# Optimization experiments

Hardware: AMD Instinct MI355X
Metric: run time of the kernel (lower is better)

Reference implementation:

```python
import jax, jax.numpy as jnp
from jax import lax
import numpy as np

K = 4            # prototypes per class: 3 kmeans centroids + 1 backbone
EPS = 0.1        # sinkhorn entropic regularization
MAX_ITER = 100
THRESH = 0.01
KM_ITERS = 10    # Lloyd iterations (replaces host-side sklearn KMeans)
HW = 28          # the original reshapes pred to 28x28, fixing n = 784


def setup_inputs():
    key = jax.random.key(0)
    k1, k2, k3, k4 = jax.random.split(key, 4)
    b, n, d, c = 32, HW * HW, 1024, 20
    return {
        "query": jax.random.normal(k1, (b, n, d), dtype=jnp.float32),
        "score": jax.random.uniform(k2, (b, n, c), dtype=jnp.float32),
        "label": jax.random.randint(k3, (b, c), 0, 2),
        "gt": jax.random.randint(k4, (b, HW, HW), 0, c + 1),
        "weights": jnp.array([1.0, 1.0, 0.0, -1.0], dtype=jnp.float32),
    }


def _assign(dq, cen, selfm):
    # dq [b,m,d], cen [b,c,j,d], selfm [b,c,m] float mask -> one-hot labels, counts
    x2 = jnp.sum(dq * dq, axis=-1)                                   # [b,m]
    d2 = (x2[:, None, :, None]
          - 2.0 * jnp.einsum('bmd,bcjd->bcmj', dq, cen)
          + jnp.sum(cen * cen, axis=-1)[:, :, None, :])              # [b,c,m,j]
    oh = jax.nn.one_hot(jnp.argmin(d2, axis=-1), cen.shape[2], dtype=dq.dtype) * selfm[..., None]
    return oh, oh.sum(axis=2)


def _sinkhorn(Km, u, v):
    # vectorized over the [b,c] pair grid, per-pair early exit as in the torch loop
    def cond(st):
        it, r, cc, done = st
        return (it < MAX_ITER) & jnp.logical_not(jnp.all(done))

    def body(st):
        it, r, cc, done = st
        r1 = u / jnp.einsum('bcnj,bcj->bcn', Km, cc)
        c1 = v / jnp.einsum('bcnj,bcn->bcj', Km, r1)
        err = jnp.mean(jnp.abs(r1 - r), axis=-1)                     # [b,c]
        r = jnp.where(done[..., None], r, r1)
        cc = jnp.where(done[..., None], cc, c1)
        done = done | (err < THRESH)
        return it + 1, r, cc, done

    st = (jnp.int32(0), jnp.ones_like(u), jnp.ones_like(v),
          jnp.zeros(Km.shape[:2], dtype=bool))
    _, r, cc, _ = lax.while_loop(cond, body, st)
    return r[..., :, None] * cc[..., None, :] * Km                   # [b,c,n,K]


def _forward(query, score, label, gt, weights):
    b, n, d = query.shape
    c = score.shape[2]
    dq, ds = query[:, ::2, :], score[:, ::2, :]                      # stride-2 downsample
    m = dq.shape[1]
    cls_assign = jnp.argmax(ds, axis=-1)                             # [b,m]
    sel = cls_assign[:, None, :] == jnp.arange(c)[None, :, None]     # [b,c,m]
    selfm = sel.astype(query.dtype)
    cnt = selfm.sum(-1)                                              # [b,c]
    valid = (label > 0) & (cnt >= K)

    # ---- masked Lloyd's k-means with k-1 = 3 clusters per (image, class) pair
    order = jnp.argsort((~sel).astype(jnp.int32), axis=-1)           # masked points first
    init_idx = order[..., :K - 1]                                    # [b,c,3]
    cen = dq[jnp.arange(b)[:, None, None], init_idx]                 # [b,c,3,d]

    def km_step(cen, _):
        oh, kcnt = _assign(dq, cen, selfm)
        sums = jnp.einsum('bmd,bcmj->bcjd', dq, oh)
        cen = jnp.where(kcnt[..., None] > 0,
                        sums / jnp.maximum(kcnt, 1.0)[..., None], cen)
        return cen, None

    cen, _ = lax.scan(km_step, cen, None, length=KM_ITERS)
    oh, kcnt = _assign(dq, cen, selfm)                               # final labels

    # ---- sort centroids by mean cluster score (descending)
    sm = ds.mean(axis=-1)                                            # [b,m]
    avg = jnp.where(kcnt > 0,
                    jnp.einsum('bm,bcmj->bcj', sm, oh) / jnp.maximum(kcnt, 1.0),
                    -jnp.inf)
    ordj = jnp.argsort(-avg, axis=-1)                                # [b,c,3]
    cen = jnp.take_along_axis(cen, ordj[..., None], axis=2)

    # ---- backbone prototype = mean over unselected downsampled tokens
    un = 1.0 - selfm
    backbone = jnp.einsum('bmd,bcm->bcd', dq, un) / jnp.maximum(m - cnt, 1.0)[..., None]
    protos = jnp.concatenate([cen, backbone[:, :, None, :]], axis=2)  # [b,c,4,d]

    # ---- OT between query[0] tokens and the 4 prototypes (original uses query[0] always)
    q0 = query[0]
    q0h = q0 / jnp.maximum(jnp.linalg.norm(q0, axis=-1, keepdims=True), 1e-12)
    ph = protos / jnp.maximum(jnp.linalg.norm(protos, axis=-1, keepdims=True), 1e-12)
    sim = jnp.einsum('nd,bcjd->bcnj', q0h, ph)                       # [b,c,n,4]
    Km = lax.stop_gradient(jnp.exp(-(1.0 - sim) / EPS))              # torch.no_grad
    u = jnp.full((b, c, n), 1.0 / n, dtype=query.dtype)
    v = jnp.full((b, c, K), 1.0 / K, dtype=query.dtype)
    T = lax.stop_gradient(_sinkhorn(Km, u, v))                       # [b,c,n,4]

    valid = valid & jnp.logical_not(jnp.any(jnp.isnan(T), axis=(2, 3)))
    pred = jnp.einsum('bcnj,j->bcn', T, weights)                     # [b,c,n]

    # ---- BCE vs gt masks (28x28 -> 28x28 bilinear resize is the identity)
    y = (gt.reshape(b, -1)[:, None, :] == (jnp.arange(c) + 1)[None, :, None]).astype(pred.dtype)
    p = jnp.clip(pred, 0.0, 1.0)
    bce = -(y * jnp.maximum(jnp.log(p), -100.0)
            + (1.0 - y) * jnp.maximum(jnp.log(1.0 - p), -100.0)).mean(axis=-1)  # [b,c]
    bce = jnp.where(valid, bce, 0.0)
    total_n = valid.sum().astype(pred.dtype)
    return bce.sum() / (total_n + 1e-4)


def reference(query, score, label, gt, weights):
    return _forward(query, score, label, gt, weights)
```

## Files before the change

kernel.cpp:

```cpp
#include <hip/hip_runtime.h>
#include <cmath>

#define BB 32
#define NN 784
#define MM 392
#define DD 1024
#define CC 20
#define JJ 3
#define KP 4
#define KM_ITERS 10
#define GMAX 64
#define SKK 3
#define NCOL (BB * CC * KP)

__global__ void k_cls(const float* __restrict__ score, int* __restrict__ cls,
                      float* __restrict__ sm, int* __restrict__ cnt) {
  int t = blockIdx.x * blockDim.x + threadIdx.x;
  if (t >= BB * MM) return;
  int b = t / MM, i = t - b * MM;
  const float* s = score + ((size_t)b * NN + 2 * i) * CC;
  float best = s[0]; int bi = 0; float acc = s[0];
  #pragma unroll
  for (int c = 1; c < CC; c++) { float v = s[c]; acc += v; if (v > best) { best = v; bi = c; } }
  cls[t] = bi;
  sm[t] = acc / (float)CC;
  atomicAdd(&cnt[b * CC + bi], 1);
}

__global__ void k_valid(const int* __restrict__ label, const int* __restrict__ cnt,
                        int* __restrict__ vlist, int* __restrict__ cpos, int* __restrict__ nvp) {
  __shared__ int sf[1024];
  int t = threadIdx.x;
  int flag = 0;
  if (t < BB * CC) flag = (label[t] > 0 && cnt[t] >= KP) ? 1 : 0;
  sf[t] = flag;
  __syncthreads();
  for (int off = 1; off < 1024; off <<= 1) {
    int v = sf[t];
    int add = (t >= off) ? sf[t - off] : 0;
    __syncthreads();
    sf[t] = v + add;
    __syncthreads();
  }
  if (t < BB * CC) {
    int pos = sf[t] - flag;
    cpos[t] = flag ? pos : -1;
    if (flag) vlist[pos] = t;
  }
  if (t == 0) *nvp = sf[BB * CC - 1];
}

__global__ __launch_bounds__(256) void k_csum(const float* __restrict__ query,
    const int* __restrict__ cls, float* __restrict__ classsum) {
  int b = blockIdx.x, ch = blockIdx.y;
  int tid = threadIdx.x, lane = tid & 63, wv = tid >> 6;
  __shared__ float acc[4][CC][64];
  __shared__ int s_cls[MM];
  #pragma unroll
  for (int c = 0; c < CC; c++) acc[wv][c][lane] = 0.f;
  for (int i = tid; i < MM; i += 256) s_cls[i] = cls[b * MM + i];
  __syncthreads();
  const float* qb = query + (size_t)b * NN * DD + ch * 64 + lane;
  int i0 = wv * 98;
  #pragma unroll 4
  for (int r = 0; r < 98; r++) {
    int i = i0 + r;
    float v = qb[(size_t)(2 * i) * DD];
    int cl = s_cls[i];
    acc[wv][cl][lane] += v;
  }
  __syncthreads();
  for (int cc = wv; cc < CC; cc += 4) {
    float s = acc[0][cc][lane] + acc[1][cc][lane] + acc[2][cc][lane] + acc[3][cc][lane];
    classsum[((size_t)(b * CC + cc)) * DD + ch * 64 + lane] = s;
  }
}

__global__ __launch_bounds__(512) void k_gram(
    const float* __restrict__ query, const int* __restrict__ cls,
    const int* __restrict__ cpos, const float* __restrict__ sm,
    float* __restrict__ ph) {
  int bc = blockIdx.x;
  if (cpos[bc] < 0) return;
  int b = bc / CC, c = bc - b * CC;
  int tid = threadIdx.x, lane = tid & 63, wv = tid >> 6;
  const float* qb = query + (size_t)b * NN * DD;
  __shared__ int s_wtot[8];
  __shared__ int s_list[GMAX];
  __shared__ __align__(16) float Xs[GMAX][132];
  __shared__ float Gl[GMAX][65];
  __shared__ float s_w[JJ][GMAX];
  __shared__ int s_rank[JJ];
  __shared__ float s_red2[6];

  int flag = 0;
  if (tid < MM) flag = (cls[b * MM + tid] == c) ? 1 : 0;
  unsigned long long msk = __ballot(flag);
  int wp = __popcll(msk & ((1ull << lane) - 1ull));
  if (lane == 0) s_wtot[wv] = __popcll(msk);
  __syncthreads();
  int off = 0, mtot = 0;
  #pragma unroll
  for (int w = 0; w < 8; w++) { int t = s_wtot[w]; if (w < wv) off += t; mtot += t; }
  int mc = mtot > GMAX ? GMAX : mtot;
  if (flag) { int pos = off + wp; if (pos < GMAX) s_list[pos] = tid; }
  __syncthreads();

  const float* pb[4] = {nullptr, nullptr, nullptr, nullptr};
  float* xd[4] = {nullptr, nullptr, nullptr, nullptr};
  #pragma unroll
  for (int s = 0; s < 4; s++) {
    int e = tid + s * 512;
    if (e < mc * 32) {
      pb[s] = qb + (size_t)(2 * s_list[e >> 5]) * DD + (e & 31) * 4;
      xd[s] = &Xs[e >> 5][(e & 31) * 4];
    }
  }

  int T = (mc + 1) >> 1;
  int ntile = T * (T + 1) / 2;
  int ti_[2], tj_[2];
  float a00[2], a01[2], a10[2], a11[2];
  #pragma unroll
  for (int s = 0; s < 2; s++) {
    ti_[s] = -1; tj_[s] = 0;
    a00[s] = 0.f; a01[s] = 0.f; a10[s] = 0.f; a11[s] = 0.f;
    int p = tid + s * 512;
    if (p < ntile) {
      int i = (int)floorf((sqrtf(8.0f * (float)p + 1.0f) - 1.0f) * 0.5f);
      while ((i + 1) * (i + 2) / 2 <= p) i++;
      while (i * (i + 1) / 2 > p) i--;
      ti_[s] = i; tj_[s] = p - i * (i + 1) / 2;
    }
  }

  float4 cur[4], nxt[4];
  #pragma unroll
  for (int s = 0; s < 4; s++) {
    cur[s] = make_float4(0.f, 0.f, 0.f, 0.f);
    nxt[s] = make_float4(0.f, 0.f, 0.f, 0.f);
    if (pb[s]) cur[s] = *(const float4*)(pb[s]);
  }
  for (int ch = 0; ch < 8; ch++) {
    __syncthreads();
    #pragma unroll
    for (int s = 0; s < 4; s++) if (pb[s]) *(float4*)xd[s] = cur[s];
    if (ch < 7) {
      #pragma unroll
      for (int s = 0; s < 4; s++) if (pb[s]) nxt[s] = *(const float4*)(pb[s] + (ch + 1) * 128);
    }
    __syncthreads();
    #pragma unroll
    for (int s = 0; s < 2; s++) {
      if (ti_[s] >= 0) {
        const float4* xr0 = (const float4*)&Xs[2 * ti_[s]][0];
        const float4* xr1 = (const float4*)&Xs[2 * ti_[s] + 1][0];
        const float4* xc0 = (const float4*)&Xs[2 * tj_[s]][0];
        const float4* xc1 = (const float4*)&Xs[2 * tj_[s] + 1][0];
        float s00 = 0.f, s01 = 0.f, s10 = 0.f, s11 = 0.f;
        #pragma unroll
        for (int kk = 0; kk < 32; kk++) {
          float4 u0 = xr0[kk], u1 = xr1[kk], w0 = xc0[kk], w1 = xc1[kk];
          s00 += u0.x * w0.x + u0.y * w0.y + u0.z * w0.z + u0.w * w0.w;
          s01 += u0.x * w1.x + u0.y * w1.y + u0.z * w1.z + u0.w * w1.w;
          s10 += u1.x * w0.x + u1.y * w0.y + u1.z * w0.z + u1.w * w0.w;
          s11 += u1.x * w1.x + u1.y * w1.y + u1.z * w1.z + u1.w * w1.w;
        }
        a00[s] += s00; a01[s] += s01; a10[s] += s10; a11[s] += s11;
      }
    }
    #pragma unroll
    for (int s = 0; s < 4; s++) cur[s] = nxt[s];
  }

  #pragma unroll
  for (int s = 0; s < 2; s++) {
    if (ti_[s] >= 0) {
      int r0 = 2 * ti_[s], r1 = r0 + 1, c0 = 2 * tj_[s], c1 = c0 + 1;
      if (r0 < mc && c0 < mc) { Gl[r0][c0] = a00[s]; Gl[c0][r0] = a00[s]; }
      if (r0 < mc && c1 < mc) { Gl[r0][c1] = a01[s]; Gl[c1][r0] = a01[s]; }
      if (r1 < mc && c0 < mc) { Gl[r1][c0] = a10[s]; Gl[c0][r1] = a10[s]; }
      if (r1 < mc && c1 < mc) { Gl[r1][c1] = a11[s]; Gl[c1][r1] = a11[s]; }
    }
  }
  __syncthreads();

  if (wv == 0) {
    bool act = lane < mc;
    float smv = act ? sm[b * MM + s_list[lane]] : 0.f;
    s_w[0][lane] = (lane == 0) ? 1.f : 0.f;
    s_w[1][lane] = (lane == 1) ? 1.f : 0.f;
    s_w[2][lane] = (lane == 2) ? 1.f : 0.f;
    int aj = 0, n0 = 0, n1 = 0, n2 = 0;
    for (int it = 0; it <= KM_ITERS; it++) {
      float h0 = 0.f, h1 = 0.f, h2 = 0.f;
      if (act) {
        for (int i = 0; i < mc; i++) {
          float g = Gl[lane][i];
          h0 += s_w[0][i] * g; h1 += s_w[1][i] * g; h2 += s_w[2][i] * g;
        }
      }
      float t0 = s_w[0][lane] * h0, t1 = s_w[1][lane] * h1, t2 = s_w[2][lane] * h2;
      for (int o = 1; o < 64; o <<= 1) {
        t0 += __shfl_xor(t0, o, 64); t1 += __shfl_xor(t1, o, 64); t2 += __shfl_xor(t2, o, 64);
      }
      float e0 = t0 - 2.f * h0, e1 = t1 - 2.f * h1, e2 = t2 - 2.f * h2;
      aj = 0; float bv = e0;
      if (e1 < bv) { bv = e1; aj = 1; }
      if (e2 < bv) { bv = e2; aj = 2; }
      n0 = __popcll(__ballot(act && aj == 0));
      n1 = __popcll(__ballot(act && aj == 1));
      n2 = __popcll(__ballot(act && aj == 2));
      if (it == KM_ITERS) break;
      if (act) {
        if (n0 > 0) s_w[0][lane] = (aj == 0) ? 1.f / (float)n0 : 0.f;
        if (n1 > 0) s_w[1][lane] = (aj == 1) ? 1.f / (float)n1 : 0.f;
        if (n2 > 0) s_w[2][lane] = (aj == 2) ? 1.f / (float)n2 : 0.f;
      }
    }
    float s0 = (act && aj == 0) ? smv : 0.f;
    float s1 = (act && aj == 1) ? smv : 0.f;
    float s2 = (act && aj == 2) ? smv : 0.f;
    for (int o = 1; o < 64; o <<= 1) {
      s0 += __shfl_xor(s0, o, 64); s1 += __shfl_xor(s1, o, 64); s2 += __shfl_xor(s2, o, 64);
    }
    if (lane == 0) {
      float avg[JJ];
      avg[0] = (n0 > 0) ? s0 / (float)n0 : -INFINITY;
      avg[1] = (n1 > 0) ? s1 / (float)n1 : -INFINITY;
      avg[2] = (n2 > 0) ? s2 / (float)n2 : -INFINITY;
      bool used[JJ] = {false, false, false};
      for (int s = 0; s < JJ; s++) {
        int bi = -1; float bv = 0.f;
        for (int j = 0; j < JJ; j++)
          if (!used[j] && (bi < 0 || avg[j] > bv)) { bi = j; bv = avg[j]; }
        used[bi] = true; s_rank[bi] = s;
      }
    }
  }
  __syncthreads();

  float4 a0 = make_float4(0.f, 0.f, 0.f, 0.f), a1 = make_float4(0.f, 0.f, 0.f, 0.f);
  int j = tid >> 7, q = tid & 127;
  if (tid < 384) {
    for (int g = 0; g < mc; g++) {
      float w = s_w[j][g];
      if (w != 0.f) {
        const float4* row = (const float4*)(qb + (size_t)(2 * s_list[g]) * DD);
        float4 v0 = row[q], v1 = row[q + 128];
        a0.x += w * v0.x; a0.y += w * v0.y; a0.z += w * v0.z; a0.w += w * v0.w;
        a1.x += w * v1.x; a1.y += w * v1.y; a1.z += w * v1.z; a1.w += w * v1.w;
      }
    }
    float ssq = a0.x * a0.x + a0.y * a0.y + a0.z * a0.z + a0.w * a0.w
              + a1.x * a1.x + a1.y * a1.y + a1.z * a1.z + a1.w * a1.w;
    #pragma unroll
    for (int o = 1; o < 64; o <<= 1) ssq += __shfl_xor(ssq, o, 64);
    if (lane == 0) s_red2[wv] = ssq;
  }
  __syncthreads();
  if (tid < 384) {
    float nrm = fmaxf(sqrtf(s_red2[2 * j] + s_red2[2 * j + 1]), 1e-12f);
    float4* dst = (float4*)(ph + ((size_t)bc * KP + s_rank[j]) * DD);
    float4 o0 = make_float4(a0.x / nrm, a0.y / nrm, a0.z / nrm, a0.w / nrm);
    float4 o1 = make_float4(a1.x / nrm, a1.y / nrm, a1.z / nrm, a1.w / nrm);
    dst[q] = o0; dst[q + 128] = o1;
  }
}

__global__ __launch_bounds__(256) void k_backbone(const float* __restrict__ classsum,
    const int* __restrict__ cpos, const int* __restrict__ cnt, float* __restrict__ ph) {
  int bc = blockIdx.x;
  if (cpos[bc] < 0) return;
  int b = bc / CC;
  int tid = threadIdx.x, lane = tid & 63, wv = tid >> 6;
  __shared__ float s_red[4];
  __shared__ float s_nrm;
  float4 ts = make_float4(0.f, 0.f, 0.f, 0.f);
  for (int c2 = 0; c2 < CC; c2++) {
    float4 v = *(const float4*)(classsum + ((size_t)(b * CC + c2)) * DD + tid * 4);
    ts.x += v.x; ts.y += v.y; ts.z += v.z; ts.w += v.w;
  }
  float4 cs = *(const float4*)(classsum + (size_t)bc * DD + tid * 4);
  float denom = fmaxf((float)(MM - cnt[bc]), 1.f);
  float4 v = make_float4((ts.x - cs.x) / denom, (ts.y - cs.y) / denom,
                         (ts.z - cs.z) / denom, (ts.w - cs.w) / denom);
  float pp = v.x * v.x + v.y * v.y + v.z * v.z + v.w * v.w;
  for (int o = 1; o < 64; o <<= 1) pp += __shfl_xor(pp, o, 64);
  if (lane == 0) s_red[wv] = pp;
  __syncthreads();
  if (tid == 0) s_nrm = fmaxf(sqrtf(s_red[0] + s_red[1] + s_red[2] + s_red[3]), 1e-12f);
  __syncthreads();
  float nrm = s_nrm;
  *(float4*)(ph + ((size_t)bc * KP + 3) * DD + tid * 4) =
      make_float4(v.x / nrm, v.y / nrm, v.z / nrm, v.w / nrm);
}

__global__ void k_q0h(const float* __restrict__ query, float* __restrict__ q0h) {
  int n = blockIdx.x;
  const float* src = query + (size_t)n * DD;
  float ss = 0.f;
  for (int k = threadIdx.x; k < DD; k += 64) { float v = src[k]; ss += v * v; }
  for (int o = 32; o > 0; o >>= 1) ss += __shfl_xor(ss, o, 64);
  float nrm = fmaxf(sqrtf(ss), 1e-12f);
  for (int k = threadIdx.x; k < DD; k += 64) q0h[(size_t)n * DD + k] = src[k] / nrm;
}

__global__ __launch_bounds__(256) void k_gemm(const float* __restrict__ A,
    const float* __restrict__ ph, const int* __restrict__ vlist,
    const int* __restrict__ nvp, float* __restrict__ P) {
  int nv4 = 4 * *nvp;
  int n0 = blockIdx.y * 64;
  if (n0 >= nv4) return;
  __shared__ float As[64][20];
  __shared__ float Bs[64][20];
  int tx = threadIdx.x & 15, ty = threadIdx.x >> 4;
  int m0 = blockIdx.x * 64;
  int s = blockIdx.z;
  int lrow = threadIdx.x >> 2;
  int lk = (threadIdx.x & 3) * 4;
  int brow = n0 + lrow;
  bool bval = brow < nv4;
  const float* Brow = ph;
  if (bval) {
    int bcc = brow >> 2;
    Brow = ph + ((size_t)vlist[bcc] * KP + (brow & 3)) * DD;
  }
  float acc[4][4] = {};
  int kbase = s * 352;
  int kend = (kbase + 352 < DD) ? (kbase + 352) : DD;
  for (int k0 = kbase; k0 < kend; k0 += 16) {
    int ar = m0 + lrow;
    float4 av = (ar < NN) ? *(const float4*)(A + (size_t)ar * DD + k0 + lk)
                          : make_float4(0.f, 0.f, 0.f, 0.f);
    *(float4*)&As[lrow][lk] = av;
    float4 bv = bval ? *(const float4*)(Brow + k0 + lk)
                     : make_float4(0.f, 0.f, 0.f, 0.f);
    *(float4*)&Bs[lrow][lk] = bv;
    __syncthreads();
    #pragma unroll
    for (int kk = 0; kk < 16; kk += 4) {
      float4 a4[4], b4[4];
      #pragma unroll
      for (int i = 0; i < 4; i++) a4[i] = *(const float4*)&As[ty * 4 + i][kk];
      #pragma unroll
      for (int j = 0; j < 4; j++) b4[j] = *(const float4*)&Bs[tx + 16 * j][kk];
      #pragma unroll
      for (int i = 0; i < 4; i++)
        #pragma unroll
        for (int j = 0; j < 4; j++) {
          acc[i][j] += a4[i].x * b4[j].x;
          acc[i][j] += a4[i].y * b4[j].y;
          acc[i][j] += a4[i].z * b4[j].z;
          acc[i][j] += a4[i].w * b4[j].w;
        }
    }
    __syncthreads();
  }
  #pragma unroll
  for (int j = 0; j < 4; j++) {
    int col = n0 + tx + 16 * j;
    float4 o4 = make_float4(acc[0][j], acc[1][j], acc[2][j], acc[3][j]);
    *(float4*)(P + ((size_t)s * NCOL + col) * NN + m0 + ty * 4) = o4;
  }
}

__global__ __launch_bounds__(256) void k_sink(const float* __restrict__ P,
    const int* __restrict__ cpos, const int* __restrict__ gt,
    const float* __restrict__ wts, float* __restrict__ bce, int* __restrict__ vld) {
  int bc = blockIdx.x; int b = bc / CC, c = bc - b * CC;
  int tid = threadIdx.x;
  if (cpos[bc] < 0) {
    if (tid == 0) { bce[bc] = 0.f; vld[bc] = 0; }
    return;
  }
  int p = cpos[bc];
  int lane = tid & 63, wv = tid >> 6;
  __shared__ float ccv[KP];
  __shared__ float wred[4][5];
  __shared__ float s_err;
  __shared__ int s_nan;
  float4 kv[4]; float rr[4];
  #pragma unroll
  for (int s4 = 0; s4 < 4; s4++) {
    int n = tid + 256 * s4;
    kv[s4] = make_float4(0.f, 0.f, 0.f, 0.f); rr[s4] = 1.f;
    if (n < NN) {
      float v[KP] = {0.f, 0.f, 0.f, 0.f};
      #pragma unroll
      for (int s = 0; s < SKK; s++)
        #pragma unroll
        for (int q = 0; q < KP; q++)
          v[q] += P[((size_t)s * NCOL + 4 * p + q) * NN + n];
      float4 o;
      o.x = expf(-(1.0f - v[0]) / 0.1f);
      o.y = expf(-(1.0f - v[1]) / 0.1f);
      o.z = expf(-(1.0f - v[2]) / 0.1f);
      o.w = expf(-(1.0f - v[3]) / 0.1f);
      kv[s4] = o;
    }
  }
  if (tid < KP) ccv[tid] = 1.f;
  if (tid == 0) s_nan = 0;
  __syncthreads();
  const float uu = 1.0f / (float)NN, vv = 1.0f / (float)KP;
  for (int it = 0; it < 100; it++) {
    float c0 = ccv[0], c1 = ccv[1], c2 = ccv[2], c3 = ccv[3];
    float dsum = 0.f, p0 = 0.f, p1 = 0.f, p2 = 0.f, p3 = 0.f;
    #pragma unroll
    for (int s4 = 0; s4 < 4; s4++) {
      int n = tid + 256 * s4;
      if (n < NN) {
        float4 k4 = kv[s4];
        float S = k4.x * c0 + k4.y * c1 + k4.z * c2 + k4.w * c3;
        float r1 = uu / S;
        dsum += fabsf(r1 - rr[s4]);
        rr[s4] = r1;
        p0 += k4.x * r1; p1 += k4.y * r1; p2 += k4.z * r1; p3 += k4.w * r1;
      }
    }
    for (int o = 32; o > 0; o >>= 1) {
      dsum += __shfl_down(dsum, o, 64);
      p0 += __shfl_down(p0, o, 64); p1 += __shfl_down(p1, o, 64);
      p2 += __shfl_down(p2, o, 64); p3 += __shfl_down(p3, o, 64);
    }
    if (lane == 0) { wred[wv][0] = dsum; wred[wv][1] = p0; wred[wv][2] = p1; wred[wv][3] = p2; wred[wv][4] = p3; }
    __syncthreads();
    if (tid == 0) {
      float d = 0.f, q0 = 0.f, q1 = 0.f, q2 = 0.f, q3 = 0.f;
      for (int w = 0; w < 4; w++) { d += wred[w][0]; q0 += wred[w][1]; q1 += wred[w][2]; q2 += wred[w][3]; q3 += wred[w][4]; }
      ccv[0] = vv / q0; ccv[1] = vv / q1; ccv[2] = vv / q2; ccv[3] = vv / q3;
      s_err = d / (float)NN;
    }
    __syncthreads();
    if (s_err < 0.01f) break;
  }
  float w0 = wts[0], w1 = wts[1], w2 = wts[2], w3 = wts[3];
  float cc0 = ccv[0], cc1 = ccv[1], cc2 = ccv[2], cc3 = ccv[3];
  float bsum = 0.f; int nanloc = 0;
  const int* gtb = gt + b * NN;
  #pragma unroll
  for (int s4 = 0; s4 < 4; s4++) {
    int n = tid + 256 * s4;
    if (n < NN) {
      float4 k4 = kv[s4];
      float rv = rr[s4];
      float T0 = rv * cc0 * k4.x, T1 = rv * cc1 * k4.y, T2 = rv * cc2 * k4.z, T3 = rv * cc3 * k4.w;
      if (T0 != T0 || T1 != T1 || T2 != T2 || T3 != T3) nanloc = 1;
      float pred = T0 * w0 + T1 * w1 + T2 * w2 + T3 * w3;
      float pcl = fminf(fmaxf(pred, 0.f), 1.f);
      float t = (gtb[n] == c + 1) ? fmaxf(logf(pcl), -100.f) : fmaxf(logf(1.f - pcl), -100.f);
      bsum += t;
    }
  }
  if (nanloc) s_nan = 1;
  for (int o = 32; o > 0; o >>= 1) bsum += __shfl_down(bsum, o, 64);
  if (lane == 0) wred[wv][0] = bsum;
  __syncthreads();
  if (tid == 0) {
    float tot = wred[0][0] + wred[1][0] + wred[2][0] + wred[3][0];
    if (s_nan) { bce[bc] = 0.f; vld[bc] = 0; }
    else { bce[bc] = -(tot / (float)NN); vld[bc] = 1; }
  }
}

__global__ void k_final(const float* __restrict__ bce, const int* __restrict__ vld,
                        float* __restrict__ out) {
  __shared__ float rs[256];
  __shared__ float rc[256];
  float s = 0.f, cv = 0.f;
  for (int t = threadIdx.x; t < BB * CC; t += 256) { s += bce[t]; cv += (float)vld[t]; }
  rs[threadIdx.x] = s; rc[threadIdx.x] = cv; __syncthreads();
  for (int o = 128; o > 0; o >>= 1) {
    if (threadIdx.x < o) { rs[threadIdx.x] += rs[threadIdx.x + o]; rc[threadIdx.x] += rc[threadIdx.x + o]; }
    __syncthreads();
  }
  if (threadIdx.x == 0) out[0] = rs[0] / (rc[0] + 0.0001f);
}

extern "C" void kernel_launch(void* const* d_in, const int* in_sizes, int n_in,
                              void* d_out, int out_size, void* d_ws, size_t ws_size,
                              hipStream_t stream) {
  (void)in_sizes; (void)n_in; (void)out_size; (void)ws_size;
  const float* query = (const float*)d_in[0];
  const float* score = (const float*)d_in[1];
  const int*   label = (const int*)d_in[2];
  const int*   gt    = (const int*)d_in[3];
  const float* wts   = (const float*)d_in[4];
  float* ws = (float*)d_ws;

  size_t off = 0;
  int* cls = (int*)(ws + off);       off += (size_t)BB * MM;
  int* cnt = (int*)(ws + off);       off += (size_t)BB * CC;
  float* sm = ws + off;              off += (size_t)BB * MM;
  int* vlist = (int*)(ws + off);     off += (size_t)BB * CC;
  int* cpos = (int*)(ws + off);      off += (size_t)BB * CC;
  int* nvp = (int*)(ws + off);       off += 16;
  float* classsum = ws + off;        off += (size_t)BB * CC * DD;
  float* ph = ws + off;              off += (size_t)BB * CC * KP * DD;
  float* q0h = ws + off;             off += (size_t)NN * DD;
  float* P = ws + off;               off += (size_t)SKK * NN * NCOL;
  float* bce = ws + off;             off += (size_t)BB * CC;
  int* vld = (int*)(ws + off);       off += (size_t)BB * CC;

  hipMemsetAsync(cnt, 0, (size_t)BB * CC * sizeof(int), stream);
  k_cls<<<(BB * MM + 255) / 256, 256, 0, stream>>>(score, cls, sm, cnt);
  k_valid<<<1, 1024, 0, stream>>>(label, cnt, vlist, cpos, nvp);
  k_csum<<<dim3(BB, 16), 256, 0, stream>>>(query, cls, classsum);
  k_gram<<<BB * CC, 512, 0, stream>>>(query, cls, cpos, sm, ph);
  k_backbone<<<BB * CC, 256, 0, stream>>>(classsum, cpos, cnt, ph);
  k_q0h<<<NN, 64, 0, stream>>>(query, q0h);
  dim3 gg((NN + 63) / 64, (BB * CC * KP) / 64, SKK);
  k_gemm<<<gg, 256, 0, stream>>>(q0h, ph, vlist, nvp, P);
  k_sink<<<BB * CC, 256, 0, stream>>>(P, cpos, gt, wts, bce, vld);
  k_final<<<1, 256, 0, stream>>>(bce, vld, (float*)d_out);
}
```

Baseline: 301.1 us.

## Move similarity GEMM to bf16 MFMA with hi/lo split for fp32 accuracy

Prototypes and normalized queries are now stored as bf16 hi/lo pairs, and the similarity GEMM is rebuilt around MFMA 16x16x32 bf16 instructions. Three MFMAs per tile (hh, hl, lh) approximate fp32 precision. The split-K over three slices and the summation of partials in the Sinkhorn kernel are removed. Each wave loads its operands straight from global memory with no LDS staging, which may limit bandwidth reuse. The final 64-row tile also reads past the 784 valid A rows without a bounds check, and the dropped lo*lo term causes small precision drift that the exp with EPS 0.1 amplifies.

```diff
diff --git a/kernel.cpp b/kernel.cpp
--- a/kernel.cpp
+++ b/kernel.cpp
@@ -10,8 +10,31 @@
 #define KP 4
 #define KM_ITERS 10
 #define GMAX 64
-#define SKK 3
 #define NCOL (BB * CC * KP)
+
+typedef __attribute__((ext_vector_type(8))) short bf16x8;
+typedef __attribute__((ext_vector_type(4))) float f32x4;
+
+__device__ inline unsigned short f2bf(float x) {
+  unsigned int u = __float_as_uint(x);
+  u += 0x7FFFu + ((u >> 16) & 1u);
+  return (unsigned short)(u >> 16);
+}
+__device__ inline float bf2f(unsigned short h) {
+  return __uint_as_float(((unsigned int)h) << 16);
+}
+__device__ inline void f2bf2(float x, unsigned short& hi, unsigned short& lo) {
+  hi = f2bf(x);
+  lo = f2bf(x - bf2f(hi));
+}
+__device__ inline void store_bf4(unsigned short* baseh, unsigned short* basel,
+                                 int idx4, float4 v) {
+  ushort4 h, l;
+  f2bf2(v.x, h.x, l.x); f2bf2(v.y, h.y, l.y);
+  f2bf2(v.z, h.z, l.z); f2bf2(v.w, h.w, l.w);
+  ((ushort4*)baseh)[idx4] = h;
+  ((ushort4*)basel)[idx4] = l;
+}
 
 __global__ void k_cls(const float* __restrict__ score, int* __restrict__ cls,
                       float* __restrict__ sm, int* __restrict__ cnt) {
@@ -79,7 +102,7 @@
 __global__ __launch_bounds__(512) void k_gram(
     const float* __restrict__ query, const int* __restrict__ cls,
     const int* __restrict__ cpos, const float* __restrict__ sm,
-    float* __restrict__ ph) {
+    unsigned short* __restrict__ phh, unsigned short* __restrict__ phl) {
   int bc = blockIdx.x;
   if (cpos[bc] < 0) return;
   int b = bc / CC, c = bc - b * CC;
@@ -261,15 +284,17 @@
   __syncthreads();
   if (tid < 384) {
     float nrm = fmaxf(sqrtf(s_red2[2 * j] + s_red2[2 * j + 1]), 1e-12f);
-    float4* dst = (float4*)(ph + ((size_t)bc * KP + s_rank[j]) * DD);
+    size_t rowoff = ((size_t)bc * KP + s_rank[j]) * DD;
     float4 o0 = make_float4(a0.x / nrm, a0.y / nrm, a0.z / nrm, a0.w / nrm);
     float4 o1 = make_float4(a1.x / nrm, a1.y / nrm, a1.z / nrm, a1.w / nrm);
-    dst[q] = o0; dst[q + 128] = o1;
+    store_bf4(phh + rowoff, phl + rowoff, q, o0);
+    store_bf4(phh + rowoff, phl + rowoff, q + 128, o1);
   }
 }
 
 __global__ __launch_bounds__(256) void k_backbone(const float* __restrict__ classsum,
-    const int* __restrict__ cpos, const int* __restrict__ cnt, float* __restrict__ ph) {
+    const int* __restrict__ cpos, const int* __restrict__ cnt,
+    unsigned short* __restrict__ phh, unsigned short* __restrict__ phl) {
   int bc = blockIdx.x;
   if (cpos[bc] < 0) return;
   int b = bc / CC;
@@ -292,76 +317,90 @@
   if (tid == 0) s_nrm = fmaxf(sqrtf(s_red[0] + s_red[1] + s_red[2] + s_red[3]), 1e-12f);
   __syncthreads();
   float nrm = s_nrm;
-  *(float4*)(ph + ((size_t)bc * KP + 3) * DD + tid * 4) =
-      make_float4(v.x / nrm, v.y / nrm, v.z / nrm, v.w / nrm);
-}
-
-__global__ void k_q0h(const float* __restrict__ query, float* __restrict__ q0h) {
+  size_t rowoff = ((size_t)bc * KP + 3) * DD;
+  store_bf4(phh + rowoff, phl + rowoff, tid,
+            make_float4(v.x / nrm, v.y / nrm, v.z / nrm, v.w / nrm));
+}
+
+__global__ void k_q0h(const float* __restrict__ query,
+                      unsigned short* __restrict__ q0hh, unsigned short* __restrict__ q0hl) {
   int n = blockIdx.x;
   const float* src = query + (size_t)n * DD;
   float ss = 0.f;
   for (int k = threadIdx.x; k < DD; k += 64) { float v = src[k]; ss += v * v; }
   for (int o = 32; o > 0; o >>= 1) ss += __shfl_xor(ss, o, 64);
   float nrm = fmaxf(sqrtf(ss), 1e-12f);
-  for (int k = threadIdx.x; k < DD; k += 64) q0h[(size_t)n * DD + k] = src[k] / nrm;
-}
-
-__global__ __launch_bounds__(256) void k_gemm(const float* __restrict__ A,
-    const float* __restrict__ ph, const int* __restrict__ vlist,
-    const int* __restrict__ nvp, float* __restrict__ P) {
+  for (int k = threadIdx.x; k < DD; k += 64) {
+    unsigned short hi, lo;
+    f2bf2(src[k] / nrm, hi, lo);
+    q0hh[(size_t)n * DD + k] = hi;
+    q0hl[(size_t)n * DD + k] = lo;
+  }
+}
+
+__global__ __launch_bounds__(64) void k_gemm(
+    const unsigned short* __restrict__ Ah, const unsigned short* __restrict__ Al,
+    const unsigned short* __restrict__ Bh, const unsigned short* __restrict__ Bl,
+    const int* __restrict__ vlist, const int* __restrict__ nvp,
+    float* __restrict__ P) {
   int nv4 = 4 * *nvp;
   int n0 = blockIdx.y * 64;
   if (n0 >= nv4) return;
-  __shared__ float As[64][20];
-  __shared__ float Bs[64][20];
-  int tx = threadIdx.x & 15, ty = threadIdx.x >> 4;
   int m0 = blockIdx.x * 64;
-  int s = blockIdx.z;
-  int lrow = threadIdx.x >> 2;
-  int lk = (threadIdx.x & 3) * 4;
-  int brow = n0 + lrow;
-  bool bval = brow < nv4;
-  const float* Brow = ph;
-  if (bval) {
-    int bcc = brow >> 2;
-    Brow = ph + ((size_t)vlist[bcc] * KP + (brow & 3)) * DD;
-  }
-  float acc[4][4] = {};
-  int kbase = s * 352;
-  int kend = (kbase + 352 < DD) ? (kbase + 352) : DD;
-  for (int k0 = kbase; k0 < kend; k0 += 16) {
-    int ar = m0 + lrow;
-    float4 av = (ar < NN) ? *(const float4*)(A + (size_t)ar * DD + k0 + lk)
-                          : make_float4(0.f, 0.f, 0.f, 0.f);
-    *(float4*)&As[lrow][lk] = av;
-    float4 bv = bval ? *(const float4*)(Brow + k0 + lk)
-                     : make_float4(0.f, 0.f, 0.f, 0.f);
-    *(float4*)&Bs[lrow][lk] = bv;
-    __syncthreads();
-    #pragma unroll
-    for (int kk = 0; kk < 16; kk += 4) {
-      float4 a4[4], b4[4];
+  int lane = threadIdx.x;
+  int kh = lane >> 4;
+  int lr = lane & 15;
+
+  const unsigned short* pa_h[4]; const unsigned short* pa_l[4];
+  #pragma unroll
+  for (int mi = 0; mi < 4; mi++) {
+    size_t o = (size_t)(m0 + mi * 16 + lr) * DD + kh * 8;
+    pa_h[mi] = Ah + o; pa_l[mi] = Al + o;
+  }
+  const unsigned short* pb_h[4]; const unsigned short* pb_l[4];
+  #pragma unroll
+  for (int ni = 0; ni < 4; ni++) {
+    int col = n0 + ni * 16 + lr;
+    int cc = (col < nv4) ? col : 0;
+    size_t o = ((size_t)vlist[cc >> 2] * KP + (cc & 3)) * DD + kh * 8;
+    pb_h[ni] = Bh + o; pb_l[ni] = Bl + o;
+  }
+
+  f32x4 acc[4][4];
+  #pragma unroll
+  for (int mi = 0; mi < 4; mi++)
+    #pragma unroll
+    for (int ni = 0; ni < 4; ni++) acc[mi][ni] = (f32x4){0.f, 0.f, 0.f, 0.f};
+
+  for (int k0 = 0; k0 < DD; k0 += 32) {
+    bf16x8 ah[4], al[4], bh[4], bl[4];
+    #pragma unroll
+    for (int i = 0; i < 4; i++) {
+      ah[i] = *(const bf16x8*)(pa_h[i] + k0);
+      al[i] = *(const bf16x8*)(pa_l[i] + k0);
+      bh[i] = *(const bf16x8*)(pb_h[i] + k0);
+      bl[i] = *(const bf16x8*)(pb_l[i] + k0);
+    }
+    #pragma unroll
+    for (int mi = 0; mi < 4; mi++)
       #pragma unroll
-      for (int i = 0; i < 4; i++) a4[i] = *(const float4*)&As[ty * 4 + i][kk];
-      #pragma unroll
-      for (int j = 0; j < 4; j++) b4[j] = *(const float4*)&Bs[tx + 16 * j][kk];
-      #pragma unroll
-      for (int i = 0; i < 4; i++)
-        #pragma unroll
-        for (int j = 0; j < 4; j++) {
-          acc[i][j] += a4[i].x * b4[j].x;
-          acc[i][j] += a4[i].y * b4[j].y;
-          acc[i][j] += a4[i].z * b4[j].z;
-          acc[i][j] += a4[i].w * b4[j].w;
-        }
-    }
-    __syncthreads();
-  }
-  #pragma unroll
-  for (int j = 0; j < 4; j++) {
-    int col = n0 + tx + 16 * j;
-    float4 o4 = make_float4(acc[0][j], acc[1][j], acc[2][j], acc[3][j]);
-    *(float4*)(P + ((size_t)s * NCOL + col) * NN + m0 + ty * 4) = o4;
+      for (int ni = 0; ni < 4; ni++) {
+        acc[mi][ni] = __builtin_amdgcn_mfma_f32_16x16x32_bf16(ah[mi], bh[ni], acc[mi][ni], 0, 0, 0);
+        acc[mi][ni] = __builtin_amdgcn_mfma_f32_16x16x32_bf16(ah[mi], bl[ni], acc[mi][ni], 0, 0, 0);
+        acc[mi][ni] = __builtin_amdgcn_mfma_f32_16x16x32_bf16(al[mi], bh[ni], acc[mi][ni], 0, 0, 0);
+      }
+  }
+
+  #pragma unroll
+  for (int ni = 0; ni < 4; ni++) {
+    int col = n0 + ni * 16 + lr;
+    #pragma unroll
+    for (int mi = 0; mi < 4; mi++) {
+      int m = m0 + mi * 16 + kh * 4;
+      if (m < NN) {
+        *(f32x4*)(P + (size_t)col * NN + m) = acc[mi][ni];
+      }
+    }
   }
 }
 
@@ -386,12 +425,10 @@
     int n = tid + 256 * s4;
     kv[s4] = make_float4(0.f, 0.f, 0.f, 0.f); rr[s4] = 1.f;
     if (n < NN) {
-      float v[KP] = {0.f, 0.f, 0.f, 0.f};
+      float v[KP];
       #pragma unroll
-      for (int s = 0; s < SKK; s++)
-        #pragma unroll
-        for (int q = 0; q < KP; q++)
-          v[q] += P[((size_t)s * NCOL + 4 * p + q) * NN + n];
+      for (int q = 0; q < KP; q++)
+        v[q] = P[((size_t)(4 * p + q)) * NN + n];
       float4 o;
       o.x = expf(-(1.0f - v[0]) / 0.1f);
       o.y = expf(-(1.0f - v[1]) / 0.1f);
@@ -490,28 +527,30 @@
   float* ws = (float*)d_ws;
 
   size_t off = 0;
-  int* cls = (int*)(ws + off);       off += (size_t)BB * MM;
-  int* cnt = (int*)(ws + off);       off += (size_t)BB * CC;
-  float* sm = ws + off;              off += (size_t)BB * MM;
-  int* vlist = (int*)(ws + off);     off += (size_t)BB * CC;
-  int* cpos = (int*)(ws + off);      off += (size_t)BB * CC;
-  int* nvp = (int*)(ws + off);       off += 16;
-  float* classsum = ws + off;        off += (size_t)BB * CC * DD;
-  float* ph = ws + off;              off += (size_t)BB * CC * KP * DD;
-  float* q0h = ws + off;             off += (size_t)NN * DD;
-  float* P = ws + off;               off += (size_t)SKK * NN * NCOL;
-  float* bce = ws + off;             off += (size_t)BB * CC;
-  int* vld = (int*)(ws + off);       off += (size_t)BB * CC;
+  int* cls = (int*)(ws + off);            off += (size_t)BB * MM;
+  int* cnt = (int*)(ws + off);            off += (size_t)BB * CC;
+  float* sm = ws + off;                   off += (size_t)BB * MM;
+  int* vlist = (int*)(ws + off);          off += (size_t)BB * CC;
+  int* cpos = (int*)(ws + off);           off += (size_t)BB * CC;
+  int* nvp = (int*)(ws + off);            off += 16;
+  float* classsum = ws + off;             off += (size_t)BB * CC * DD;
+  unsigned short* q0hh = (unsigned short*)(ws + off);  off += (size_t)NN * DD / 2;
+  unsigned short* q0hl = (unsigned short*)(ws + off);  off += (size_t)NN * DD / 2;
+  unsigned short* phh = (unsigned short*)(ws + off);   off += (size_t)BB * CC * KP * DD / 2;
+  unsigned short* phl = (unsigned short*)(ws + off);   off += (size_t)BB * CC * KP * DD / 2;
+  float* P = ws + off;                    off += (size_t)NCOL * NN;
+  float* bce = ws + off;                  off += (size_t)BB * CC;
+  int* vld = (int*)(ws + off);            off += (size_t)BB * CC;
 
   hipMemsetAsync(cnt, 0, (size_t)BB * CC * sizeof(int), stream);
   k_cls<<<(BB * MM + 255) / 256, 256, 0, stream>>>(score, cls, sm, cnt);
   k_valid<<<1, 1024, 0, stream>>>(label, cnt, vlist, cpos, nvp);
   k_csum<<<dim3(BB, 16), 256, 0, stream>>>(query, cls, classsum);
-  k_gram<<<BB * CC, 512, 0, stream>>>(query, cls, cpos, sm, ph);
-  k_backbone<<<BB * CC, 256, 0, stream>>>(classsum, cpos, cnt, ph);
-  k_q0h<<<NN, 64, 0, stream>>>(query, q0h);
-  dim3 gg((NN + 63) / 64, (BB * CC * KP) / 64, SKK);
-  k_gemm<<<gg, 256, 0, stream>>>(q0h, ph, vlist, nvp, P);
+  k_gram<<<BB * CC, 512, 0, stream>>>(query, cls, cpos, sm, phh, phl);
+  k_backbone<<<BB * CC, 256, 0, stream>>>(classsum, cpos, cnt, phh, phl);
+  k_q0h<<<NN, 64, 0, stream>>>(query, q0hh, q0hl);
+  dim3 gg((NN + 63) / 64, NCOL / 64);
+  k_gemm<<<gg, 64, 0, stream>>>(q0hh, q0hl, phh, phl, vlist, nvp, P);
   k_sink<<<BB * CC, 256, 0, stream>>>(P, cpos, gt, wts, bce, vld);
   k_final<<<1, 256, 0, stream>>>(bce, vld, (float*)d_out);
 }
```

Result: no change. 301.0 us (-0.0%).
